# Kernel optimization log

Hardware: AMD Instinct MI355X
Metric: run time of the kernel (lower is better)

The kernel has to match this reference:

```python
import jax, jax.numpy as jnp
import numpy as np

EPS = 1e-5  # torch BatchNorm1d default eps
N_CONV = 3


def _bn_train(x, gamma, beta):
    # training-mode BatchNorm1d over axis 0 (biased variance, like torch)
    m = jnp.mean(x, axis=0)
    v = jnp.var(x, axis=0)
    return (x - m) * jax.lax.rsqrt(v + EPS) * gamma + beta


def _conv_layer(x, nbr_fea, nbr_idx, W, b, g1, b1, g2, b2):
    # x: (N, D); nbr_fea: (N, M, F); nbr_idx: (N, M)
    N, M = nbr_idx.shape
    D = x.shape[1]
    atom_nbr = x[nbr_idx]                                  # gather (N, M, D)
    total = jnp.concatenate(
        [jnp.broadcast_to(x[:, None, :], (N, M, D)), atom_nbr, nbr_fea], axis=2
    )                                                      # (N, M, 2D+F)
    z = jnp.einsum('nmf,of->nmo', total, W) + b            # (N, M, 2D)
    z = _bn_train(z.reshape(N * M, 2 * D), g1, b1).reshape(N, M, 2 * D)
    filt, core = jnp.split(z, 2, axis=2)
    summed = jnp.sum(jax.nn.sigmoid(filt) * jax.nn.softplus(core), axis=1)  # (N, D)
    summed = _bn_train(summed, g2, b2)
    return jax.nn.softplus(x + summed)


def setup_inputs() -> dict:
    key = jax.random.key(0)
    ks = jax.random.split(key, 16)
    N, M = 32768, 12
    ORIG, NBR, D = 92, 41, 64
    B, NA = 512, 64  # 512 crystals x 64 atoms = N
    s = 0.05
    inp = {
        'atom_fea': jax.random.normal(ks[0], (N, ORIG), jnp.float32),
        'nbr_fea': jax.random.normal(ks[1], (N, M, NBR), jnp.float32),
        'nbr_fea_idx': jax.random.randint(ks[2], (N, M), 0, N),
        'crystal_atom_idx': jnp.arange(N).reshape(B, NA),
        'embed_W': jax.random.normal(ks[3], (D, ORIG), jnp.float32) * s,
        'conv_W': jax.random.normal(ks[4], (N_CONV, 2 * D, 2 * D + NBR), jnp.float32) * s,
        'conv_b': jax.random.normal(ks[5], (N_CONV, 2 * D), jnp.float32) * s,
        'bn1_g': jnp.ones((N_CONV, 2 * D), jnp.float32),
        'bn1_b': jnp.zeros((N_CONV, 2 * D), jnp.float32),
        'bn2_g': jnp.ones((N_CONV, D), jnp.float32),
        'bn2_b': jnp.zeros((N_CONV, D), jnp.float32),
        'bil_W': jax.random.normal(ks[6], (6, D, D), jnp.float32) * s,
        'bil_b': jax.random.normal(ks[7], (6,), jnp.float32) * s,
        'fc1_W': jax.random.normal(ks[8], (6, 6), jnp.float32) * s,
        'fc1_b': jax.random.normal(ks[9], (6,), jnp.float32) * s,
        'fca_W': jax.random.normal(ks[10], (ORIG, D), jnp.float32) * s,
        'fca_b': jax.random.normal(ks[11], (ORIG,), jnp.float32) * s,
    }
    return inp


def reference(atom_fea, nbr_fea, nbr_fea_idx, crystal_atom_idx,
              embed_W, conv_W, conv_b, bn1_g, bn1_b, bn2_g, bn2_b,
              bil_W, bil_b, fc1_W, fc1_b, fca_W, fca_b):
    # embedding (no bias)
    x = atom_fea @ embed_W.T                                # (N, D)
    for i in range(N_CONV):
        x = _conv_layer(x, nbr_fea, nbr_fea_idx,
                        conv_W[i], conv_b[i], bn1_g[i], bn1_b[i], bn2_g[i], bn2_b[i])
    B, NA = crystal_atom_idx.shape
    f = x[crystal_atom_idx]                                 # (B, NA, D) per-crystal embs
    # bilinear over all (i, j) pairs per crystal: edge[b,i,j,o]
    edge = jnp.einsum('bid,odk,bjk->bijo', f, bil_W, f) + bil_b
    edge = edge @ fc1_W.T + fc1_b
    edge = jax.nn.log_softmax(edge, axis=-1)
    edge = edge.reshape(B, NA * NA, 6)                      # stacked edge_prob_list
    atom_out = f @ fca_W.T + fca_b                          # stacked atom_feature_list
    return edge, atom_out
```

## Files before the change

kernel.cpp:

```cpp
#include <hip/hip_runtime.h>
#include <math.h>

#define BN_EPS 1e-5f

typedef unsigned short u16;
typedef unsigned short ushort8_t __attribute__((ext_vector_type(8)));

__device__ __forceinline__ float sp_f(float x){
    return fmaxf(x, 0.0f) + __logf(1.0f + __expf(-fabsf(x)));
}
__device__ __forceinline__ float sig_f(float x){
    return __builtin_amdgcn_rcpf(1.0f + __expf(-x));
}
__device__ __forceinline__ u16 f2bf(float f){
    unsigned int u = __float_as_uint(f);
    unsigned int r = (u + 0x7fffu + ((u >> 16) & 1u)) >> 16;
    return (u16)r;
}
__device__ __forceinline__ float bf2f(u16 h){
    return __uint_as_float(((unsigned int)h) << 16);
}

__global__ __launch_bounds__(256) void k_embed(const float* __restrict__ af,
                                               const float* __restrict__ ew,
                                               float* __restrict__ x){
    __shared__ float ew_s[64*93];
    __shared__ float af_s[16*92];
    const int t = threadIdx.x;
    for (int s = t; s < 64*92; s += 256){ int d = s/92, k = s - d*92; ew_s[d*93+k] = ew[s]; }
    const int n0 = blockIdx.x * 16;
    for (int s = t; s < 16*92; s += 256) af_s[s] = af[(size_t)n0*92 + s];
    __syncthreads();
    const int rl = t >> 6, d = t & 63;
    #pragma unroll
    for (int rep = 0; rep < 4; rep++){
        const int row = rep*4 + rl;
        float acc = 0.0f;
        for (int k = 0; k < 92; k++) acc += af_s[row*92+k] * ew_s[d*93+k];
        x[(size_t)(n0+row)*64 + d] = acc;
    }
}

__global__ __launch_bounds__(256) void k_nbr2bf(const float* __restrict__ nbr,
                                                u16* __restrict__ nbrb){
    const int tot4 = 16121856/4;
    for (int i = blockIdx.x*256 + threadIdx.x; i < tot4; i += 2048*256){
        float4 v = *reinterpret_cast<const float4*>(nbr + (size_t)i*4);
        ushort4 o; o.x=f2bf(v.x); o.y=f2bf(v.y); o.z=f2bf(v.z); o.w=f2bf(v.w);
        *reinterpret_cast<ushort4*>(nbrb + (size_t)i*4) = o;
    }
}

__global__ void k_transpose_w(const float* __restrict__ W, float* __restrict__ WT){
    int idx = blockIdx.x*256 + threadIdx.x;
    if (idx < 169*128){ int fp = idx >> 7, o = idx & 127; WT[idx] = W[o*169 + fp]; }
}

__global__ __launch_bounds__(256) void k_a12(const float* __restrict__ x,
                                             const float* __restrict__ WT,
                                             const float* __restrict__ bias,
                                             const float* __restrict__ summed,
                                             const float* __restrict__ kab2,
                                             int apply,
                                             u16* __restrict__ A1, u16* __restrict__ A2,
                                             float* __restrict__ xout){
    __shared__ float xs[16*64];
    const int t = threadIdx.x;
    const int n0 = blockIdx.x * 16;
    for (int s = t; s < 16*64; s += 256){
        float xv = x[(size_t)n0*64 + s];
        if (apply){
            const int d = s & 63;
            xv = sp_f(xv + summed[(size_t)n0*64 + s]*kab2[d] + kab2[64+d]);
            xout[(size_t)n0*64 + s] = xv;
        }
        xs[s] = xv;
    }
    __syncthreads();
    const int o = t & 127, rh = t >> 7;
    float a1[8], a2[8];
    const float b = bias[o];
    #pragma unroll
    for (int r = 0; r < 8; r++){ a1[r] = b; a2[r] = 0.0f; }
    for (int d = 0; d < 64; d++){
        const float w1 = WT[d*128 + o];
        const float w2 = WT[(64+d)*128 + o];
        #pragma unroll
        for (int r = 0; r < 8; r++){
            const float xv = xs[(rh*8+r)*64 + d];
            a1[r] += xv*w1; a2[r] += xv*w2;
        }
    }
    #pragma unroll
    for (int r = 0; r < 8; r++){
        const int n = n0 + rh*8 + r;
        A1[(size_t)n*128 + o] = f2bf(a1[r]);
        A2[(size_t)n*128 + o] = f2bf(a2[r]);
    }
}

__global__ __launch_bounds__(256, 4) void k_conv(
    const u16* __restrict__ nbrb, const int* __restrict__ nidx,
    const u16* __restrict__ A1, const u16* __restrict__ A2,
    const float* __restrict__ WT, u16* __restrict__ z, float* __restrict__ partials)
{
    __shared__ float w3s[41*132];
    __shared__ float nts[41*72];
    __shared__ int   idxs[192];
    __shared__ float st[256];
    const int t = threadIdx.x;
    st[t] = 0.0f;
    for (int s = t; s < 41*128; s += 256){
        int k = s >> 7, o = s & 127;
        w3s[k*132 + o] = WT[16384 + s];
    }
    const int e0b = blockIdx.x * 192;
    if (t < 192) idxs[t] = nidx[e0b + t];
    const int t32 = t & 31, eg = t >> 5;
    float ssum[4] = {0,0,0,0}, ssq[4] = {0,0,0,0};
    for (int it = 0; it < 3; it++){
        const int e0 = e0b + it*64;
        __syncthreads();
        ushort4 a1v[8], a2v[8];
        #pragma unroll
        for (int el = 0; el < 8; el++){
            const int e = e0 + eg*8 + el;
            const int n = e / 12;
            const int g = idxs[it*64 + eg*8 + el];
            a1v[el] = *reinterpret_cast<const ushort4*>(A1 + (size_t)n*128 + t32*4);
            a2v[el] = *reinterpret_cast<const ushort4*>(A2 + (size_t)g*128 + t32*4);
        }
        for (int s4 = t; s4 < 656; s4 += 256){
            ushort4 v = *reinterpret_cast<const ushort4*>(nbrb + (size_t)e0*41 + s4*4);
            int s = s4*4;
            { int e = s/41,   k = s   - e*41; nts[k*72 + e] = bf2f(v.x); }
            { int e = (s+1)/41, k = s+1 - e*41; nts[k*72 + e] = bf2f(v.y); }
            { int e = (s+2)/41, k = s+2 - e*41; nts[k*72 + e] = bf2f(v.z); }
            { int e = (s+3)/41, k = s+3 - e*41; nts[k*72 + e] = bf2f(v.w); }
        }
        __syncthreads();
        float acc[8][4];
        #pragma unroll
        for (int el = 0; el < 8; el++){
            acc[el][0] = bf2f(a1v[el].x) + bf2f(a2v[el].x);
            acc[el][1] = bf2f(a1v[el].y) + bf2f(a2v[el].y);
            acc[el][2] = bf2f(a1v[el].z) + bf2f(a2v[el].z);
            acc[el][3] = bf2f(a1v[el].w) + bf2f(a2v[el].w);
        }
        for (int k = 0; k < 41; k++){
            const float4 w  = *reinterpret_cast<const float4*>(w3s + k*132 + t32*4);
            const float4 na = *reinterpret_cast<const float4*>(nts + k*72 + eg*8);
            const float4 nb = *reinterpret_cast<const float4*>(nts + k*72 + eg*8 + 4);
            acc[0][0] += na.x*w.x; acc[0][1] += na.x*w.y; acc[0][2] += na.x*w.z; acc[0][3] += na.x*w.w;
            acc[1][0] += na.y*w.x; acc[1][1] += na.y*w.y; acc[1][2] += na.y*w.z; acc[1][3] += na.y*w.w;
            acc[2][0] += na.z*w.x; acc[2][1] += na.z*w.y; acc[2][2] += na.z*w.z; acc[2][3] += na.z*w.w;
            acc[3][0] += na.w*w.x; acc[3][1] += na.w*w.y; acc[3][2] += na.w*w.z; acc[3][3] += na.w*w.w;
            acc[4][0] += nb.x*w.x; acc[4][1] += nb.x*w.y; acc[4][2] += nb.x*w.z; acc[4][3] += nb.x*w.w;
            acc[5][0] += nb.y*w.x; acc[5][1] += nb.y*w.y; acc[5][2] += nb.y*w.z; acc[5][3] += nb.y*w.w;
            acc[6][0] += nb.z*w.x; acc[6][1] += nb.z*w.y; acc[6][2] += nb.z*w.z; acc[6][3] += nb.z*w.w;
            acc[7][0] += nb.w*w.x; acc[7][1] += nb.w*w.y; acc[7][2] += nb.w*w.z; acc[7][3] += nb.w*w.w;
        }
        #pragma unroll
        for (int el = 0; el < 8; el++){
            const int e = e0 + eg*8 + el;
            ushort4 pk;
            pk.x = f2bf(acc[el][0]); pk.y = f2bf(acc[el][1]);
            pk.z = f2bf(acc[el][2]); pk.w = f2bf(acc[el][3]);
            *reinterpret_cast<ushort4*>(z + (size_t)e*128 + t32*4) = pk;
            #pragma unroll
            for (int j = 0; j < 4; j++){
                ssum[j] += acc[el][j];
                ssq[j]  += acc[el][j]*acc[el][j];
            }
        }
    }
    #pragma unroll
    for (int j = 0; j < 4; j++){
        atomicAdd(&st[t32*4 + j], ssum[j]);
        atomicAdd(&st[128 + t32*4 + j], ssq[j]);
    }
    __syncthreads();
    partials[(size_t)blockIdx.x*256 + t] = st[t];
}

__global__ __launch_bounds__(256) void k_bn_reduce(const float* __restrict__ partials, int nblk, int C,
        float invcount, const float* __restrict__ g, const float* __restrict__ bt,
        float* __restrict__ kab){
    const int c = blockIdx.x;
    const int t = threadIdx.x;
    float s = 0.0f, q = 0.0f;
    for (int b = t; b < nblk; b += 256){
        s += partials[(size_t)b*2*C + c];
        q += partials[(size_t)b*2*C + C + c];
    }
    __shared__ float ls[256], lq[256];
    ls[t] = s; lq[t] = q; __syncthreads();
    for (int off = 128; off > 0; off >>= 1){
        if (t < off){ ls[t] += ls[t+off]; lq[t] += lq[t+off]; }
        __syncthreads();
    }
    if (t == 0){
        const float mean = ls[0]*invcount;
        const float var  = lq[0]*invcount - mean*mean;
        const float rstd = rsqrtf(var + BN_EPS);
        const float ka = g[c]*rstd;
        kab[c]     = ka;
        kab[C + c] = bt[c] - mean*ka;
    }
}

__global__ __launch_bounds__(256, 6) void k_gate(const u16* __restrict__ z,
        const float* __restrict__ kab, float* __restrict__ summed,
        float* __restrict__ partials){
    const int t = threadIdx.x;
    const int a = t >> 4, q = t & 15;
    const int n = blockIdx.x*16 + a;
    const int d0 = q*4;
    float kaf[4], kbf[4], kac[4], kbc[4];
    #pragma unroll
    for (int j = 0; j < 4; j++){
        const int d = d0 + j;
        kaf[j] = kab[d];      kbf[j] = kab[128 + d];
        kac[j] = kab[64 + d]; kbc[j] = kab[192 + d];
    }
    const u16* zp = z + (size_t)n*1536 + d0;
    float acc[4] = {0,0,0,0};
    #pragma unroll 4
    for (int m = 0; m < 12; m++){
        ushort4 fv = *reinterpret_cast<const ushort4*>(zp + m*128);
        ushort4 cv = *reinterpret_cast<const ushort4*>(zp + m*128 + 64);
        acc[0] += sig_f(bf2f(fv.x)*kaf[0]+kbf[0]) * sp_f(bf2f(cv.x)*kac[0]+kbc[0]);
        acc[1] += sig_f(bf2f(fv.y)*kaf[1]+kbf[1]) * sp_f(bf2f(cv.y)*kac[1]+kbc[1]);
        acc[2] += sig_f(bf2f(fv.z)*kaf[2]+kbf[2]) * sp_f(bf2f(cv.z)*kac[2]+kbc[2]);
        acc[3] += sig_f(bf2f(fv.w)*kaf[3]+kbf[3]) * sp_f(bf2f(cv.w)*kac[3]+kbc[3]);
    }
    float4 sv; sv.x=acc[0]; sv.y=acc[1]; sv.z=acc[2]; sv.w=acc[3];
    *reinterpret_cast<float4*>(summed + (size_t)n*64 + d0) = sv;
    float sq[4];
    #pragma unroll
    for (int j = 0; j < 4; j++) sq[j] = acc[j]*acc[j];
    #pragma unroll
    for (int j = 0; j < 4; j++){
        acc[j] += __shfl_xor(acc[j], 16); acc[j] += __shfl_xor(acc[j], 32);
        sq[j]  += __shfl_xor(sq[j],  16); sq[j]  += __shfl_xor(sq[j],  32);
    }
    __shared__ float st[128];
    if (t < 128) st[t] = 0.0f;
    __syncthreads();
    if ((t & 48) == 0){
        #pragma unroll
        for (int j = 0; j < 4; j++){
            atomicAdd(&st[d0 + j], acc[j]);
            atomicAdd(&st[64 + d0 + j], sq[j]);
        }
    }
    __syncthreads();
    if (t < 128) partials[(size_t)blockIdx.x*128 + t] = st[t];
}

__global__ __launch_bounds__(256) void k_gather_upd(const float* __restrict__ x,
        const float* __restrict__ summed, const float* __restrict__ kab,
        const int* __restrict__ cidx, float* __restrict__ f){
    const int idx = blockIdx.x*256 + threadIdx.x;
    const int r = idx >> 4, q = idx & 15;
    const int src = cidx[r];
    const int d0 = q*4;
    float4 xv = *reinterpret_cast<const float4*>(x + (size_t)src*64 + d0);
    float4 sv = *reinterpret_cast<const float4*>(summed + (size_t)src*64 + d0);
    float4 o;
    o.x = sp_f(xv.x + sv.x*kab[d0+0] + kab[64+d0+0]);
    o.y = sp_f(xv.y + sv.y*kab[d0+1] + kab[64+d0+1]);
    o.z = sp_f(xv.z + sv.z*kab[d0+2] + kab[64+d0+2]);
    o.w = sp_f(xv.w + sv.w*kab[d0+3] + kab[64+d0+3]);
    *reinterpret_cast<float4*>(f + (size_t)r*64 + d0) = o;
}

__global__ __launch_bounds__(256) void k_edge(
    const float* __restrict__ f, const float* __restrict__ bilW,
    const float* __restrict__ bilb, const float* __restrict__ fc1W,
    const float* __restrict__ fc1b, float* __restrict__ out)
{
    __shared__ float fs[64*68];
    __shared__ float ws[64*68];
    __shared__ float ts[64*68];
    __shared__ float cb[48];
    const int t = threadIdx.x;
    const int b = blockIdx.x;
    for (int s = t; s < 4096; s += 256){
        int i = s >> 6, d = s & 63;
        fs[i*68 + d] = f[(size_t)b*4096 + s];
    }
    if (t < 6){ cb[t] = bilb[t]; cb[6+t] = fc1b[t]; }
    if (t < 36) cb[12+t] = fc1W[t];
    const int ti = t >> 4, tj = t & 15;
    float acc[6][4][4];
    #pragma unroll
    for (int o = 0; o < 6; o++)
        #pragma unroll
        for (int a = 0; a < 4; a++)
            #pragma unroll
            for (int c = 0; c < 4; c++) acc[o][a][c] = 0.0f;

    #pragma unroll
    for (int o = 0; o < 6; o++){
        __syncthreads();
        for (int s = t; s < 4096; s += 256){
            int d = s >> 6, k = s & 63;
            ws[k*68 + d] = bilW[o*4096 + s];
        }
        __syncthreads();
        float T[4][4];
        #pragma unroll
        for (int a = 0; a < 4; a++)
            #pragma unroll
            for (int c = 0; c < 4; c++) T[a][c] = 0.0f;
        for (int d = 0; d < 64; d += 4){
            float4 fv[4], wv[4];
            #pragma unroll
            for (int a = 0; a < 4; a++) fv[a] = *reinterpret_cast<const float4*>(&fs[(a*16+ti)*68 + d]);
            #pragma unroll
            for (int c = 0; c < 4; c++) wv[c] = *reinterpret_cast<const float4*>(&ws[(c*16+tj)*68 + d]);
            #pragma unroll
            for (int a = 0; a < 4; a++)
                #pragma unroll
                for (int c = 0; c < 4; c++)
                    T[a][c] += fv[a].x*wv[c].x + fv[a].y*wv[c].y + fv[a].z*wv[c].z + fv[a].w*wv[c].w;
        }
        __syncthreads();
        #pragma unroll
        for (int a = 0; a < 4; a++)
            #pragma unroll
            for (int c = 0; c < 4; c++)
                ts[(a*16+ti)*68 + c*16+tj] = T[a][c];
        __syncthreads();
        for (int k = 0; k < 64; k += 4){
            float4 ta[4], fb[4];
            #pragma unroll
            for (int a = 0; a < 4; a++) ta[a] = *reinterpret_cast<const float4*>(&ts[(a*16+ti)*68 + k]);
            #pragma unroll
            for (int c = 0; c < 4; c++) fb[c] = *reinterpret_cast<const float4*>(&fs[(c*16+tj)*68 + k]);
            #pragma unroll
            for (int a = 0; a < 4; a++)
                #pragma unroll
                for (int c = 0; c < 4; c++)
                    acc[o][a][c] += ta[a].x*fb[c].x + ta[a].y*fb[c].y + ta[a].z*fb[c].z + ta[a].w*fb[c].w;
        }
    }
    #pragma unroll
    for (int a = 0; a < 4; a++){
        const int i = a*16 + ti;
        #pragma unroll
        for (int c = 0; c < 4; c++){
            const int j = c*16 + tj;
            float v[6];
            float mx = -1e30f;
            #pragma unroll
            for (int p = 0; p < 6; p++){
                float s = cb[6+p];
                #pragma unroll
                for (int o = 0; o < 6; o++) s += cb[12 + p*6 + o] * (acc[o][a][c] + cb[o]);
                v[p] = s;
                mx = fmaxf(mx, s);
            }
            float se = 0.0f;
            #pragma unroll
            for (int p = 0; p < 6; p++) se += __expf(v[p] - mx);
            const float lse = __logf(se) + mx;
            float* op = out + ((size_t)b*4096 + i*64 + j)*6;
            #pragma unroll
            for (int p = 0; p < 6; p++) op[p] = v[p] - lse;
        }
    }
}

__global__ __launch_bounds__(256) void k_atomout(const float* __restrict__ f,
        const float* __restrict__ fcaW, const float* __restrict__ fcab,
        float* __restrict__ out){
    __shared__ float wt[64*93];
    const int t = threadIdx.x;
    for (int s = t; s < 5888; s += 256){ int c = s >> 6, d = s & 63; wt[d*93 + c] = fcaW[s]; }
    __syncthreads();
    const int rl = t >> 5, c32 = t & 31;
    for (int rep = 0; rep < 4; rep++){
        const int r = blockIdx.x*32 + rep*8 + rl;
        float acc0 = fcab[c32], acc1 = fcab[c32+32];
        float acc2 = (c32 < 28) ? fcab[c32+64] : 0.0f;
        const float* fr = f + (size_t)r*64;
        for (int d = 0; d < 64; d++){
            const float fv = fr[d];
            const float* wrow = wt + d*93;
            acc0 += fv*wrow[c32];
            acc1 += fv*wrow[c32+32];
            if (c32 < 28) acc2 += fv*wrow[c32+64];
        }
        float* op = out + (size_t)r*92;
        op[c32] = acc0; op[c32+32] = acc1;
        if (c32 < 28) op[c32+64] = acc2;
    }
}

extern "C" void kernel_launch(void* const* d_in, const int* in_sizes, int n_in,
                              void* d_out, int out_size, void* d_ws, size_t ws_size,
                              hipStream_t stream)
{
    (void)in_sizes; (void)n_in; (void)out_size; (void)ws_size;
    const float* atom_fea = (const float*)d_in[0];
    const float* nbr_fea  = (const float*)d_in[1];
    const int*   nbr_idx  = (const int*)  d_in[2];
    const int*   cry_idx  = (const int*)  d_in[3];
    const float* embed_W  = (const float*)d_in[4];
    const float* conv_W   = (const float*)d_in[5];
    const float* conv_b   = (const float*)d_in[6];
    const float* bn1_g    = (const float*)d_in[7];
    const float* bn1_b    = (const float*)d_in[8];
    const float* bn2_g    = (const float*)d_in[9];
    const float* bn2_b    = (const float*)d_in[10];
    const float* bil_W    = (const float*)d_in[11];
    const float* bil_b    = (const float*)d_in[12];
    const float* fc1_W    = (const float*)d_in[13];
    const float* fc1_b    = (const float*)d_in[14];
    const float* fca_W    = (const float*)d_in[15];
    const float* fca_b    = (const float*)d_in[16];
    float* out = (float*)d_out;

    char* wsb = (char*)d_ws;
    float* x      = (float*)(wsb + 0);
    float* summed = (float*)(wsb + 8388608);
    float* WT     = (float*)(wsb + 16777216);
    float* part1  = (float*)(wsb + 16863744);
    float* kab1   = (float*)(wsb + 19485184);
    float* kab2   = (float*)(wsb + 19486208);
    u16*   A1     = (u16*)  (wsb + 19486720);
    u16*   A2     = (u16*)  (wsb + 27875328);
    u16*   nbrb   = (u16*)  (wsb + 36263936);
    u16*   z      = (u16*)  (wsb + 68507648);
    float* fpool  = (float*)A1;
    float* part2  = part1;

    k_embed<<<2048, 256, 0, stream>>>(atom_fea, embed_W, x);
    k_nbr2bf<<<2048, 256, 0, stream>>>(nbr_fea, nbrb);

    for (int L = 0; L < 3; L++){
        k_transpose_w<<<85, 256, 0, stream>>>(conv_W + L*128*169, WT);
        k_a12<<<2048, 256, 0, stream>>>(x, WT, conv_b + L*128, summed, kab2,
                                        (L > 0) ? 1 : 0, A1, A2, x);
        k_conv<<<2048, 256, 0, stream>>>(nbrb, nbr_idx, A1, A2, WT, z, part1);
        k_bn_reduce<<<128, 256, 0, stream>>>(part1, 2048, 128, 1.0f/393216.0f,
                                             bn1_g + L*128, bn1_b + L*128, kab1);
        k_gate<<<2048, 256, 0, stream>>>(z, kab1, summed, part2);
        k_bn_reduce<<<64, 256, 0, stream>>>(part2, 2048, 64, 1.0f/32768.0f,
                                            bn2_g + L*64, bn2_b + L*64, kab2);
    }

    k_gather_upd<<<2048, 256, 0, stream>>>(x, summed, kab2, cry_idx, fpool);
    k_edge<<<512, 256, 0, stream>>>(fpool, bil_W, bil_b, fc1_W, fc1_b, out);
    k_atomout<<<1024, 256, 0, stream>>>(fpool, fca_W, fca_b, out + 12582912);
}
```

Measured before the change: 759.6 us.

## Use bf16 MFMA for neighbor-feature GEMM in conv and store summed as bf16

Rewrites the per-edge neighbor-feature projection in k_conv to use MFMA 16x16x32 bf16 instructions. It works on 128-edge tiles with K zero-padded to 64 and XOR-swizzled LDS layouts, and a pre-swizzled bf16 weight copy is produced in k_transpose_w. The A1/A2 gather-add and the BN statistics move into a separate epilogue pass through LDS. The summed buffer is also stored in bf16 to halve its traffic, at the cost of extra rounding error. Zero-padding K from 41 to 64 wastes some MFMA work, and the per-element LDS atomics in the epilogue may add contention.

New measurement: 2.036 ms. 168% more time.

```diff
diff --git a/kernel.cpp b/kernel.cpp
--- a/kernel.cpp
+++ b/kernel.cpp
@@ -4,7 +4,8 @@
 #define BN_EPS 1e-5f
 
 typedef unsigned short u16;
-typedef unsigned short ushort8_t __attribute__((ext_vector_type(8)));
+typedef short s16x8 __attribute__((ext_vector_type(8)));
+typedef float f32x4 __attribute__((ext_vector_type(4)));
 
 __device__ __forceinline__ float sp_f(float x){
     return fmaxf(x, 0.0f) + __logf(1.0f + __expf(-fabsf(x)));
@@ -51,15 +52,30 @@
     }
 }
 
-__global__ void k_transpose_w(const float* __restrict__ W, float* __restrict__ WT){
-    int idx = blockIdx.x*256 + threadIdx.x;
-    if (idx < 169*128){ int fp = idx >> 7, o = idx & 127; WT[idx] = W[o*169 + fp]; }
+__global__ void k_transpose_w(const float* __restrict__ W, float* __restrict__ WT,
+                              u16* __restrict__ w3tb){
+    const int idx = blockIdx.x*256 + threadIdx.x;
+    if (idx < 21632){
+        const int fp = idx >> 7, o = idx & 127;
+        const float w = W[o*169 + fp];
+        WT[idx] = w;
+        if (fp >= 128){
+            const int k = fp - 128;
+            const int g = k >> 3, p = k & 7;
+            w3tb[o*64 + ((g ^ (o&7))<<3) + p] = f2bf(w);
+        }
+    } else if (idx < 24576){
+        const int idx2 = idx - 21632;
+        const int o = idx2 / 23, k = 41 + idx2 % 23;
+        const int g = k >> 3, p = k & 7;
+        w3tb[o*64 + ((g ^ (o&7))<<3) + p] = 0;
+    }
 }
 
 __global__ __launch_bounds__(256) void k_a12(const float* __restrict__ x,
                                              const float* __restrict__ WT,
                                              const float* __restrict__ bias,
-                                             const float* __restrict__ summed,
+                                             const u16* __restrict__ summedb,
                                              const float* __restrict__ kab2,
                                              int apply,
                                              u16* __restrict__ A1, u16* __restrict__ A2,
@@ -71,7 +87,8 @@
         float xv = x[(size_t)n0*64 + s];
         if (apply){
             const int d = s & 63;
-            xv = sp_f(xv + summed[(size_t)n0*64 + s]*kab2[d] + kab2[64+d]);
+            const float sv = bf2f(summedb[(size_t)n0*64 + s]);
+            xv = sp_f(xv + sv*kab2[d] + kab2[64+d]);
             xout[(size_t)n0*64 + s] = xv;
         }
         xs[s] = xv;
@@ -102,82 +119,108 @@
 __global__ __launch_bounds__(256, 4) void k_conv(
     const u16* __restrict__ nbrb, const int* __restrict__ nidx,
     const u16* __restrict__ A1, const u16* __restrict__ A2,
-    const float* __restrict__ WT, u16* __restrict__ z, float* __restrict__ partials)
+    const u16* __restrict__ w3tb, u16* __restrict__ z, float* __restrict__ partials)
 {
-    __shared__ float w3s[41*132];
-    __shared__ float nts[41*72];
-    __shared__ int   idxs[192];
+    __shared__ char smem[35840];
     __shared__ float st[256];
+    u16* ab = (u16*)smem;
+    u16* bb = (u16*)(smem + 16384);
+    u16* zb = (u16*)smem;
     const int t = threadIdx.x;
     st[t] = 0.0f;
-    for (int s = t; s < 41*128; s += 256){
-        int k = s >> 7, o = s & 127;
-        w3s[k*132 + o] = WT[16384 + s];
-    }
-    const int e0b = blockIdx.x * 192;
-    if (t < 192) idxs[t] = nidx[e0b + t];
-    const int t32 = t & 31, eg = t >> 5;
-    float ssum[4] = {0,0,0,0}, ssq[4] = {0,0,0,0};
-    for (int it = 0; it < 3; it++){
-        const int e0 = e0b + it*64;
-        __syncthreads();
-        ushort4 a1v[8], a2v[8];
-        #pragma unroll
-        for (int el = 0; el < 8; el++){
-            const int e = e0 + eg*8 + el;
-            const int n = e / 12;
-            const int g = idxs[it*64 + eg*8 + el];
-            a1v[el] = *reinterpret_cast<const ushort4*>(A1 + (size_t)n*128 + t32*4);
-            a2v[el] = *reinterpret_cast<const ushort4*>(A2 + (size_t)g*128 + t32*4);
-        }
-        for (int s4 = t; s4 < 656; s4 += 256){
-            ushort4 v = *reinterpret_cast<const ushort4*>(nbrb + (size_t)e0*41 + s4*4);
-            int s = s4*4;
-            { int e = s/41,   k = s   - e*41; nts[k*72 + e] = bf2f(v.x); }
-            { int e = (s+1)/41, k = s+1 - e*41; nts[k*72 + e] = bf2f(v.y); }
-            { int e = (s+2)/41, k = s+2 - e*41; nts[k*72 + e] = bf2f(v.z); }
-            { int e = (s+3)/41, k = s+3 - e*41; nts[k*72 + e] = bf2f(v.w); }
-        }
-        __syncthreads();
-        float acc[8][4];
-        #pragma unroll
-        for (int el = 0; el < 8; el++){
-            acc[el][0] = bf2f(a1v[el].x) + bf2f(a2v[el].x);
-            acc[el][1] = bf2f(a1v[el].y) + bf2f(a2v[el].y);
-            acc[el][2] = bf2f(a1v[el].z) + bf2f(a2v[el].z);
-            acc[el][3] = bf2f(a1v[el].w) + bf2f(a2v[el].w);
-        }
-        for (int k = 0; k < 41; k++){
-            const float4 w  = *reinterpret_cast<const float4*>(w3s + k*132 + t32*4);
-            const float4 na = *reinterpret_cast<const float4*>(nts + k*72 + eg*8);
-            const float4 nb = *reinterpret_cast<const float4*>(nts + k*72 + eg*8 + 4);
-            acc[0][0] += na.x*w.x; acc[0][1] += na.x*w.y; acc[0][2] += na.x*w.z; acc[0][3] += na.x*w.w;
-            acc[1][0] += na.y*w.x; acc[1][1] += na.y*w.y; acc[1][2] += na.y*w.z; acc[1][3] += na.y*w.w;
-            acc[2][0] += na.z*w.x; acc[2][1] += na.z*w.y; acc[2][2] += na.z*w.z; acc[2][3] += na.z*w.w;
-            acc[3][0] += na.w*w.x; acc[3][1] += na.w*w.y; acc[3][2] += na.w*w.z; acc[3][3] += na.w*w.w;
-            acc[4][0] += nb.x*w.x; acc[4][1] += nb.x*w.y; acc[4][2] += nb.x*w.z; acc[4][3] += nb.x*w.w;
-            acc[5][0] += nb.y*w.x; acc[5][1] += nb.y*w.y; acc[5][2] += nb.y*w.z; acc[5][3] += nb.y*w.w;
-            acc[6][0] += nb.z*w.x; acc[6][1] += nb.z*w.y; acc[6][2] += nb.z*w.z; acc[6][3] += nb.z*w.w;
-            acc[7][0] += nb.w*w.x; acc[7][1] += nb.w*w.y; acc[7][2] += nb.w*w.z; acc[7][3] += nb.w*w.w;
-        }
-        #pragma unroll
-        for (int el = 0; el < 8; el++){
-            const int e = e0 + eg*8 + el;
-            ushort4 pk;
-            pk.x = f2bf(acc[el][0]); pk.y = f2bf(acc[el][1]);
-            pk.z = f2bf(acc[el][2]); pk.w = f2bf(acc[el][3]);
-            *reinterpret_cast<ushort4*>(z + (size_t)e*128 + t32*4) = pk;
-            #pragma unroll
-            for (int j = 0; j < 4; j++){
-                ssum[j] += acc[el][j];
-                ssq[j]  += acc[el][j]*acc[el][j];
+    const int e0 = blockIdx.x * 128;
+
+    #pragma unroll
+    for (int i = 0; i < 4; i++){
+        const int off = (i*256 + t) * 8;
+        *reinterpret_cast<float4*>(bb + off) =
+            *reinterpret_cast<const float4*>(w3tb + off);
+    }
+    {
+        float4 z4; z4.x = 0.f; z4.y = 0.f; z4.z = 0.f; z4.w = 0.f;
+        #pragma unroll
+        for (int i = 0; i < 4; i++)
+            *reinterpret_cast<float4*>(ab + (i*256 + t)*8) = z4;
+    }
+    __syncthreads();
+    for (int s = t; s < 128*41; s += 256){
+        const int e = s / 41, k = s - e*41;
+        const int g = k >> 3, p = k & 7;
+        ab[e*64 + ((g ^ (e&7))<<3) + p] = nbrb[(size_t)e0*41 + s];
+    }
+    __syncthreads();
+
+    const int wid = t >> 6, l = t & 63;
+    const int wm = wid >> 1, wn = wid & 1;
+    const int lrow = l & 15, lk = l >> 4;
+    f32x4 acc[4][4];
+    #pragma unroll
+    for (int m = 0; m < 4; m++)
+        #pragma unroll
+        for (int n = 0; n < 4; n++)
+            acc[m][n] = (f32x4){0.f, 0.f, 0.f, 0.f};
+    #pragma unroll
+    for (int kk = 0; kk < 2; kk++){
+        const int g = kk*4 + lk;
+        s16x8 af[4], bf[4];
+        #pragma unroll
+        for (int m = 0; m < 4; m++){
+            const int r = wm*64 + m*16 + lrow;
+            af[m] = *reinterpret_cast<const s16x8*>(ab + r*64 + ((g ^ (r&7))<<3));
+        }
+        #pragma unroll
+        for (int n = 0; n < 4; n++){
+            const int c = wn*64 + n*16 + lrow;
+            bf[n] = *reinterpret_cast<const s16x8*>(bb + c*64 + ((g ^ (c&7))<<3));
+        }
+        #pragma unroll
+        for (int m = 0; m < 4; m++)
+            #pragma unroll
+            for (int n = 0; n < 4; n++)
+                acc[m][n] = __builtin_amdgcn_mfma_f32_16x16x32_bf16(af[m], bf[n], acc[m][n], 0, 0, 0);
+    }
+    __syncthreads();
+
+    #pragma unroll
+    for (int m = 0; m < 4; m++){
+        #pragma unroll
+        for (int n = 0; n < 4; n++){
+            const int c = wn*64 + n*16 + lrow;
+            #pragma unroll
+            for (int r4 = 0; r4 < 4; r4++){
+                const int r = wm*64 + m*16 + lk*4 + r4;
+                zb[r*140 + c] = f2bf(acc[m][n][r4]);
             }
         }
     }
-    #pragma unroll
-    for (int j = 0; j < 4; j++){
-        atomicAdd(&st[t32*4 + j], ssum[j]);
-        atomicAdd(&st[128 + t32*4 + j], ssq[j]);
+    __syncthreads();
+
+    {
+        const int e = t >> 1, half = t & 1;
+        const int ge = e0 + e;
+        const int n_atom = ge / 12;
+        const int gnb = nidx[ge];
+        const u16* a1p = A1 + (size_t)n_atom*128 + half*64;
+        const u16* a2p = A2 + (size_t)gnb*128 + half*64;
+        u16* zp = z + (size_t)ge*128 + half*64;
+        const int cbase = half*64;
+        #pragma unroll
+        for (int jg = 0; jg < 16; jg++){
+            ushort4 zv = *reinterpret_cast<const ushort4*>(zb + e*140 + cbase + jg*4);
+            ushort4 b1 = *reinterpret_cast<const ushort4*>(a1p + jg*4);
+            ushort4 b2 = *reinterpret_cast<const ushort4*>(a2p + jg*4);
+            const float o0 = bf2f(zv.x) + bf2f(b1.x) + bf2f(b2.x);
+            const float o1 = bf2f(zv.y) + bf2f(b1.y) + bf2f(b2.y);
+            const float o2 = bf2f(zv.z) + bf2f(b1.z) + bf2f(b2.z);
+            const float o3 = bf2f(zv.w) + bf2f(b1.w) + bf2f(b2.w);
+            ushort4 ov; ov.x = f2bf(o0); ov.y = f2bf(o1); ov.z = f2bf(o2); ov.w = f2bf(o3);
+            *reinterpret_cast<ushort4*>(zp + jg*4) = ov;
+            const int c = cbase + jg*4;
+            atomicAdd(&st[c+0], o0); atomicAdd(&st[128+c+0], o0*o0);
+            atomicAdd(&st[c+1], o1); atomicAdd(&st[128+c+1], o1*o1);
+            atomicAdd(&st[c+2], o2); atomicAdd(&st[128+c+2], o2*o2);
+            atomicAdd(&st[c+3], o3); atomicAdd(&st[128+c+3], o3*o3);
+        }
     }
     __syncthreads();
     partials[(size_t)blockIdx.x*256 + t] = st[t];
@@ -210,7 +253,7 @@
 }
 
 __global__ __launch_bounds__(256, 6) void k_gate(const u16* __restrict__ z,
-        const float* __restrict__ kab, float* __restrict__ summed,
+        const float* __restrict__ kab, u16* __restrict__ summedb,
         float* __restrict__ partials){
     const int t = threadIdx.x;
     const int a = t >> 4, q = t & 15;
@@ -234,8 +277,8 @@
         acc[2] += sig_f(bf2f(fv.z)*kaf[2]+kbf[2]) * sp_f(bf2f(cv.z)*kac[2]+kbc[2]);
         acc[3] += sig_f(bf2f(fv.w)*kaf[3]+kbf[3]) * sp_f(bf2f(cv.w)*kac[3]+kbc[3]);
     }
-    float4 sv; sv.x=acc[0]; sv.y=acc[1]; sv.z=acc[2]; sv.w=acc[3];
-    *reinterpret_cast<float4*>(summed + (size_t)n*64 + d0) = sv;
+    ushort4 sv; sv.x = f2bf(acc[0]); sv.y = f2bf(acc[1]); sv.z = f2bf(acc[2]); sv.w = f2bf(acc[3]);
+    *reinterpret_cast<ushort4*>(summedb + (size_t)n*64 + d0) = sv;
     float sq[4];
     #pragma unroll
     for (int j = 0; j < 4; j++) sq[j] = acc[j]*acc[j];
@@ -259,19 +302,19 @@
 }
 
 __global__ __launch_bounds__(256) void k_gather_upd(const float* __restrict__ x,
-        const float* __restrict__ summed, const float* __restrict__ kab,
+        const u16* __restrict__ summedb, const float* __restrict__ kab,
         const int* __restrict__ cidx, float* __restrict__ f){
     const int idx = blockIdx.x*256 + threadIdx.x;
     const int r = idx >> 4, q = idx & 15;
     const int src = cidx[r];
     const int d0 = q*4;
     float4 xv = *reinterpret_cast<const float4*>(x + (size_t)src*64 + d0);
-    float4 sv = *reinterpret_cast<const float4*>(summed + (size_t)src*64 + d0);
+    ushort4 s4 = *reinterpret_cast<const ushort4*>(summedb + (size_t)src*64 + d0);
     float4 o;
-    o.x = sp_f(xv.x + sv.x*kab[d0+0] + kab[64+d0+0]);
-    o.y = sp_f(xv.y + sv.y*kab[d0+1] + kab[64+d0+1]);
-    o.z = sp_f(xv.z + sv.z*kab[d0+2] + kab[64+d0+2]);
-    o.w = sp_f(xv.w + sv.w*kab[d0+3] + kab[64+d0+3]);
+    o.x = sp_f(xv.x + bf2f(s4.x)*kab[d0+0] + kab[64+d0+0]);
+    o.y = sp_f(xv.y + bf2f(s4.y)*kab[d0+1] + kab[64+d0+1]);
+    o.z = sp_f(xv.z + bf2f(s4.z)*kab[d0+2] + kab[64+d0+2]);
+    o.w = sp_f(xv.w + bf2f(s4.w)*kab[d0+3] + kab[64+d0+3]);
     *reinterpret_cast<float4*>(f + (size_t)r*64 + d0) = o;
 }
 
@@ -424,35 +467,36 @@
     float* out = (float*)d_out;
 
     char* wsb = (char*)d_ws;
-    float* x      = (float*)(wsb + 0);
-    float* summed = (float*)(wsb + 8388608);
-    float* WT     = (float*)(wsb + 16777216);
-    float* part1  = (float*)(wsb + 16863744);
-    float* kab1   = (float*)(wsb + 19485184);
-    float* kab2   = (float*)(wsb + 19486208);
-    u16*   A1     = (u16*)  (wsb + 19486720);
-    u16*   A2     = (u16*)  (wsb + 27875328);
-    u16*   nbrb   = (u16*)  (wsb + 36263936);
-    u16*   z      = (u16*)  (wsb + 68507648);
-    float* fpool  = (float*)A1;
-    float* part2  = part1;
+    float* x       = (float*)(wsb + 0);
+    u16*   summedb = (u16*)  (wsb + 8388608);
+    float* WT      = (float*)(wsb + 12582912);
+    u16*   w3tb    = (u16*)  (wsb + 12669952);
+    float* kab1    = (float*)(wsb + 12719104);
+    float* kab2    = (float*)(wsb + 12720128);
+    float* part1   = (float*)(wsb + 12721152);
+    u16*   A1      = (u16*)  (wsb + 15866880);
+    u16*   A2      = (u16*)  (wsb + 24255488);
+    u16*   nbrb    = (u16*)  (wsb + 32644096);
+    u16*   z       = (u16*)  (wsb + 64887808);
+    float* fpool   = (float*)A1;
+    float* part2   = part1;
 
     k_embed<<<2048, 256, 0, stream>>>(atom_fea, embed_W, x);
     k_nbr2bf<<<2048, 256, 0, stream>>>(nbr_fea, nbrb);
 
     for (int L = 0; L < 3; L++){
-        k_transpose_w<<<85, 256, 0, stream>>>(conv_W + L*128*169, WT);
-        k_a12<<<2048, 256, 0, stream>>>(x, WT, conv_b + L*128, summed, kab2,
+        k_transpose_w<<<96, 256, 0, stream>>>(conv_W + L*128*169, WT, w3tb + L*8192);
+        k_a12<<<2048, 256, 0, stream>>>(x, WT, conv_b + L*128, summedb, kab2,
                                         (L > 0) ? 1 : 0, A1, A2, x);
-        k_conv<<<2048, 256, 0, stream>>>(nbrb, nbr_idx, A1, A2, WT, z, part1);
-        k_bn_reduce<<<128, 256, 0, stream>>>(part1, 2048, 128, 1.0f/393216.0f,
+        k_conv<<<3072, 256, 0, stream>>>(nbrb, nbr_idx, A1, A2, w3tb + L*8192, z, part1);
+        k_bn_reduce<<<128, 256, 0, stream>>>(part1, 3072, 128, 1.0f/393216.0f,
                                              bn1_g + L*128, bn1_b + L*128, kab1);
-        k_gate<<<2048, 256, 0, stream>>>(z, kab1, summed, part2);
+        k_gate<<<2048, 256, 0, stream>>>(z, kab1, summedb, part2);
         k_bn_reduce<<<64, 256, 0, stream>>>(part2, 2048, 64, 1.0f/32768.0f,
                                             bn2_g + L*64, bn2_b + L*64, kab2);
     }
 
-    k_gather_upd<<<2048, 256, 0, stream>>>(x, summed, kab2, cry_idx, fpool);
+    k_gather_upd<<<2048, 256, 0, stream>>>(x, summedb, kab2, cry_idx, fpool);
     k_edge<<<512, 256, 0, stream>>>(fpool, bil_W, bil_b, fc1_W, fc1_b, out);
     k_atomout<<<1024, 256, 0, stream>>>(fpool, fca_W, fca_b, out + 12582912);
 }
```
